# Optimization experiments

Hardware: AMD Instinct MI355X
Metric: run time of the kernel (lower is better)

The kernel has to match this reference:

```python
import jax, jax.numpy as jnp
import numpy as np

NLAT_IN, NLON_IN = 360, 720
NLAT_OUT, NLON_OUT = 180, 360
KERNEL_SIZE = 3
THETA_CUTOFF = KERNEL_SIZE * np.pi / NLAT_IN  # default theta_cutoff
B, C = 2, 64


def _cc_lats_weights(n):
    # Clenshaw-Curtis quadrature on [-1,1] (torch-harmonics 'equiangular' grid);
    # latitudes (colatitude) = arccos(nodes) = pi*k/(n-1) in [0, pi].
    N = n - 1
    theta = np.pi * np.arange(n) / N
    w = np.ones(n)
    for j in range(1, N // 2 + 1):
        b = 1.0 if 2 * j == N else 2.0
        w -= b * np.cos(2.0 * j * theta) / (4.0 * j * j - 1.0)
    w *= 2.0 / N
    w[0] *= 0.5
    w[-1] *= 0.5
    return theta, w


def _precompute_psi():
    # Mirrors _precompute_convolution_tensor + _compute_support_vals_isotropic.
    d_theta = THETA_CUTOFF / KERNEL_SIZE
    lats_in, _ = _cc_lats_weights(NLAT_IN)
    lats_out, _ = _cc_lats_weights(NLAT_OUT)
    phis = np.linspace(0.0, 2.0 * np.pi, NLON_IN)
    alpha = -lats_in[None, :, None].astype(np.float32)   # [1, H, 1]
    beta = phis[None, None, :].astype(np.float32)        # [1, 1, W]
    gamma = lats_out[:, None, None].astype(np.float32)   # [T, 1, 1]
    z = np.cos(alpha) * np.cos(gamma) - np.cos(beta) * np.sin(alpha) * np.sin(gamma)
    with np.errstate(invalid="ignore"):
        theta = np.arccos(z)  # [T, H, W]; nan where |z|>1 (excluded by mask, as in torch)
    segs, lats, lons, vals = [], [], [], []
    for ik in range(KERNEL_SIZE):
        itheta = ik * d_theta
        with np.errstate(invalid="ignore"):
            mask = (np.abs(theta - itheta) < d_theta) & (theta < THETA_CUTOFF)
        t_idx, h_idx, w_idx = np.nonzero(mask)
        segs.append(ik * NLAT_OUT + t_idx)  # fused (kernel, nlat_out) segment id
        lats.append(h_idx)
        lons.append(w_idx)
        vals.append(1.0 - np.abs(theta[mask] - itheta) / d_theta)
    return (np.concatenate(segs).astype(np.int32),
            np.concatenate(lats).astype(np.int32),
            np.concatenate(lons).astype(np.int32),
            np.concatenate(vals).astype(np.float32))


def setup_inputs() -> dict:
    key = jax.random.key(0)
    x = jax.random.normal(key, (B, C, NLAT_IN, NLON_IN), dtype=jnp.float32)
    _, wgl = _cc_lats_weights(NLAT_IN)
    quad_weights = jnp.asarray(2.0 * np.pi * wgl[:, None] / NLON_IN, dtype=jnp.float32)
    seg, lat, lon, val = _precompute_psi()
    return {"x": x, "quad_weights": quad_weights,
            "psi_seg": jnp.asarray(seg), "psi_lat": jnp.asarray(lat),
            "psi_lon": jnp.asarray(lon), "psi_val": jnp.asarray(val)}


def reference(x, quad_weights, psi_seg, psi_lat, psi_lon, psi_val):
    # out[b,c,k,t,p] = sum_{(k,t,h,w) in psi} val * qw[h] * x[b,c,h,(w-(p+1)*s) mod W]
    Bx, Cx, H, W = x.shape
    scale = W // NLON_OUT  # longitudinal shift per output longitude (torch.roll step)
    xw = (quad_weights * x).reshape(Bx * Cx, H, W)  # [BC, H, W]
    num_seg = KERNEL_SIZE * NLAT_OUT

    def step(carry, p):
        cols = (psi_lon - (p + 1) * scale) % W                 # rolled longitude per nnz
        g = xw[:, psi_lat, cols] * psi_val                     # [BC, nnz] gather + scale
        out_p = jax.ops.segment_sum(g.T, psi_seg, num_segments=num_seg)  # [K*T, BC]
        return carry, out_p

    _, ys = jax.lax.scan(step, None, jnp.arange(NLON_OUT))     # [P, K*T, BC]
    out = ys.transpose(2, 1, 0).reshape(Bx, Cx, KERNEL_SIZE, NLAT_OUT, NLON_OUT)
    return out
```

## Files before the change

### kernel.cpp

```cpp
#include <hip/hip_runtime.h>


#define NLAT_IN  360
#define NLON_IN  720
#define NLAT_OUT 180
#define NLON_OUT 360
#define KSIZE    3
#define NSEG     (KSIZE * NLAT_OUT)
#define CHW      (NLAT_IN * NLON_IN)
#define BCTOT    128
#define G        4
#define NBCG     (BCTOT / G)
#define MAXR     2
#define PH       10
#define NTHREADS 256
#define SLOTS    432
#define MIRROR   (SLOTS - NLON_OUT)
#define ROWB     (SLOTS * 16)
#define SWI      3

typedef float v2f __attribute__((ext_vector_type(2)));

__device__ __forceinline__ void PKF(v2f& a, v2f x, v2f c) {
    asm("v_pk_fma_f32 %0, %1, %2, %0" : "+v"(a) : "v"(x), "v"(c));
}


__global__ void prep1_kernel(const int* __restrict__ seg, const int* __restrict__ lat,
                             const float* __restrict__ val, int nnz,
                             int* __restrict__ ptrh, int* __restrict__ hbase,
                             int* __restrict__ hlast, int* __restrict__ flags) {
    int idx = blockIdx.x * blockDim.x + threadIdx.x;
    if (idx >= NSEG * PH) return;
    int s = idx / PH, j = idx - s * PH;
    int lo = 0, hi = nnz;
    while (lo < hi) { int m = (lo + hi) >> 1; if (seg[m] < s) lo = m + 1; else hi = m; }
    int e0 = lo;
    lo = e0; hi = nnz;
    while (lo < hi) { int m = (lo + hi) >> 1; if (seg[m] < s + 1) lo = m + 1; else hi = m; }
    int e1 = lo;
    if (e0 >= e1) {
        ptrh[idx] = e0; flags[idx] = 0;
        if (j == 0) { hbase[s] = 1 << 28; hlast[s] = -(1 << 28); }
        return;
    }
    int hb = lat[e0];
    if (j == 0) { hbase[s] = hb; hlast[s] = lat[e1 - 1]; }
    int a;
    { int tg = hb + j; lo = e0; hi = e1;
      while (lo < hi) { int m = (lo + hi) >> 1; if (lat[m] < tg) lo = m + 1; else hi = m; }
      a = lo; }
    ptrh[idx] = a;
    int f = 0;
    if (j < PH - 1) {
        int tg = hb + j + 1; lo = a; hi = e1;
        while (lo < hi) { int m = (lo + hi) >> 1; if (lat[m] < tg) lo = m + 1; else hi = m; }
        int b = lo;
        if (b - a == NLON_IN) {
            float v0 = val[a], v1 = val[a + 240], v2 = val[a + 480];
            float d = fmaxf(fabsf(v0 - v1), fmaxf(fabsf(v0 - v2), fabsf(v1 - v2)));
            f = (d < 1e-5f) ? 1 : 0;
        }
    }
    flags[idx] = f;
}

__global__ void cf_kernel(const int* __restrict__ lat, const float* __restrict__ val,
                          const float* __restrict__ qw, int nnz, float* __restrict__ cfb) {
    int e = blockIdx.x * blockDim.x + threadIdx.x;
    if (e < nnz) cfb[e] = val[e] * qw[lat[e]];
}

__global__ void runs_kernel(const int* __restrict__ lon, const int* __restrict__ ptrh,
                            const int* __restrict__ flags,
                            int* __restrict__ runcnt, uint2* __restrict__ runslab) {
    const int idx  = blockIdx.x * 4 + (threadIdx.x >> 6);
    if (idx >= NSEG * PH) return;
    const int lane = threadIdx.x & 63;
    const int j = idx % PH;
    int runbase = 0;
    if (j < PH - 1) {
        const int a = ptrh[idx], b = ptrh[idx + 1];
        if (b > a && !flags[idx]) {
            for (int c = a; c < b; c += 64) {
                const int e = c + lane;
                const bool active = e < b;
                const int w   = active ? lon[e] : 0;
                const int wm1 = (active && e > a) ? lon[e - 1] : -99;
                const bool isStart = active && (lane == 0 || w != wm1 + 1);
                const unsigned long long mask = __ballot(isStart);
                if (isStart) {
                    const int cnt = min(64, b - c);
                    unsigned long long hv = (mask >> lane) >> 1;
                    const int len = hv ? __ffsll((long long)hv) : (cnt - lane);
                    const int cidx = __popcll(mask & ((1ull << lane) - 1ull));
                    const int s0 = ((w >> 1) + NLON_OUT - 1) % NLON_OUT;
                    runslab[a + runbase + cidx] = make_uint2(
                        (unsigned)e, (unsigned)(s0 | ((w & 1) << 9) | (len << 11)));
                }
                runbase += __popcll(mask);
            }
        }
    }
    if (lane == 0) runcnt[idx] = runbase;
}


__global__ __launch_bounds__(NTHREADS) void disco_kernel(
    const float* __restrict__ x,
    const float* __restrict__ cfb,
    const uint2* __restrict__ runslab,
    const int*   __restrict__ runcnt,
    const int*   __restrict__ ptrh,
    const int*   __restrict__ hbase,
    const int*   __restrict__ hlast,
    const int*   __restrict__ flags,
    float*       __restrict__ out)
{
    __shared__ float4 ldsx[MAXR * 2][SLOTS];
    __shared__ v2f    accbuf[120][6];

    const int tid      = threadIdx.x;
    const int lane     = tid & 63;
    const int wpair    = tid >> 7;
    const int pairlane = tid & 127;
    const int pid      = (pairlane < 120) ? pairlane : pairlane - 120;
    const int p0       = 3 * pid;
    const int bc0      = blockIdx.x * G;
    const int ty       = blockIdx.y;
    const int t        = (ty & 1) ? (NLAT_OUT - 1 - (ty >> 1)) : (ty >> 1);
    const int s        = blockIdx.z * NLAT_OUT + t;
    const int hb = hbase[s], hl = hlast[s];

    v2f a0l = {0.f, 0.f}, a0h = a0l, a1l = a0l, a1h = a0l, a2l = a0l, a2h = a0l;
    const char* lb = (const char*)&ldsx[0][0];

    float2 sv0[4], sv1[4], sv2[4];
    const float* xb = x + (size_t)bc0 * CHW;

#define LOADW(R0)                                                              \
    {                                                                          \
        {   const int idx_ = tid;                     \
            const int rr_ = idx_ >= 360;                                       \
            const int m_  = idx_ - 360 * rr_;                                  \
            const int row_ = min((R0) + rr_, hl);                              \
            const float* xr_ = xb + (size_t)row_ * NLON_IN + 2 * m_;           \
            sv0[0] = *(const float2*)(xr_);                                    \
            sv0[1] = *(const float2*)(xr_ + CHW);                              \
            sv0[2] = *(const float2*)(xr_ + 2 * CHW);                          \
            sv0[3] = *(const float2*)(xr_ + 3 * CHW);                          \
        }                                                                      \
        {   const int idx_ = tid + 256;               \
            const int rr_ = idx_ >= 360;                                       \
            const int m_  = idx_ - 360 * rr_;                                  \
            const int row_ = min((R0) + rr_, hl);                              \
            const float* xr_ = xb + (size_t)row_ * NLON_IN + 2 * m_;           \
            sv1[0] = *(const float2*)(xr_);                                    \
            sv1[1] = *(const float2*)(xr_ + CHW);                              \
            sv1[2] = *(const float2*)(xr_ + 2 * CHW);                          \
            sv1[3] = *(const float2*)(xr_ + 3 * CHW);                          \
        }                                                                      \
        if (tid < 208) {                                 \
            const int idx_ = tid + 512;                                        \
            const int rr_ = 1;                                                 \
            const int m_  = idx_ - 360;                                        \
            const int row_ = min((R0) + rr_, hl);                              \
            const float* xr_ = xb + (size_t)row_ * NLON_IN + 2 * m_;           \
            sv2[0] = *(const float2*)(xr_);                                    \
            sv2[1] = *(const float2*)(xr_ + CHW);                              \
            sv2[2] = *(const float2*)(xr_ + 2 * CHW);                          \
            sv2[3] = *(const float2*)(xr_ + 3 * CHW);                          \
        }                                                                      \
    }

#define WRITEW()                                                               \
    {                                                                          \
        {   const int idx_ = tid;                                              \
            const int rr_ = idx_ >= 360;                                       \
            const int m_  = idx_ - 360 * rr_;                                  \
            const float4 ev_ = {sv0[0].x, sv0[1].x, sv0[2].x, sv0[3].x};       \
            const float4 ov_ = {sv0[0].y, sv0[1].y, sv0[2].y, sv0[3].y};       \
            ldsx[2 * rr_ + 0][m_] = ev_;                                       \
            ldsx[2 * rr_ + 1][m_] = ov_;                                       \
            if (m_ < MIRROR) {                                                 \
                ldsx[2 * rr_ + 0][NLON_OUT + m_] = ev_;                        \
                ldsx[2 * rr_ + 1][NLON_OUT + m_] = ov_;                        \
            }                                                                  \
        }                                                                      \
        {   const int idx_ = tid + 256;                                        \
            const int rr_ = idx_ >= 360;                                       \
            const int m_  = idx_ - 360 * rr_;                                  \
            const float4 ev_ = {sv1[0].x, sv1[1].x, sv1[2].x, sv1[3].x};       \
            const float4 ov_ = {sv1[0].y, sv1[1].y, sv1[2].y, sv1[3].y};       \
            ldsx[2 * rr_ + 0][m_] = ev_;                                       \
            ldsx[2 * rr_ + 1][m_] = ov_;                                       \
            if (m_ < MIRROR) {                                                 \
                ldsx[2 * rr_ + 0][NLON_OUT + m_] = ev_;                        \
                ldsx[2 * rr_ + 1][NLON_OUT + m_] = ov_;                        \
            }                                                                  \
        }                                                                      \
        if (tid < 208) {                                                       \
            const int m_ = tid + 512 - 360;                                    \
            const float4 ev_ = {sv2[0].x, sv2[1].x, sv2[2].x, sv2[3].x};       \
            const float4 ov_ = {sv2[0].y, sv2[1].y, sv2[2].y, sv2[3].y};       \
            ldsx[2][m_] = ev_;                                                 \
            ldsx[3][m_] = ov_;                                                 \
            if (m_ < MIRROR) {                                                 \
                ldsx[2][NLON_OUT + m_] = ev_;                                  \
                ldsx[3][NLON_OUT + m_] = ov_;                                  \
            }                                                                  \
        }                                                                      \
    }

    if (hb <= hl) {
        LOADW(hb);
        for (int r0 = hb; r0 <= hl; r0 += MAXR) {
            const int rn = min(MAXR, hl - r0 + 1);
            __syncthreads();
            WRITEW();
            if (r0 + MAXR <= hl) LOADW(r0 + MAXR);
            __syncthreads();
            for (int r = 0; r < rn; ++r) {
                const int j = (r0 + r) - hb;
                if (j < 0 || j >= PH - 1) continue;
                if ((j & 1) != wpair) continue;
                const int idx = s * PH + j;
                const int a = ptrh[idx], b = ptrh[idx + 1];
                if (a >= b) continue;
                const int rp0 = (j & 1) * 2;
                if (flags[idx]) {
                    float4 v = {0.f, 0.f, 0.f, 0.f};
                    for (int m = lane; m < NLON_OUT; m += 64) {
                        const float4 u0 = ldsx[rp0][m], u1 = ldsx[rp0 + 1][m];
                        v.x += u0.x + u1.x; v.y += u0.y + u1.y;
                        v.z += u0.z + u1.z; v.w += u0.w + u1.w;
                    }
#pragma unroll
                    for (int o = 32; o >= 1; o >>= 1) {
                        v.x += __shfl_xor(v.x, o); v.y += __shfl_xor(v.y, o);
                        v.z += __shfl_xor(v.z, o); v.w += __shfl_xor(v.w, o);
                    }
                    const float cf = cfb[a];
                    a0l.x = fmaf(cf, v.x, a0l.x); a0l.y = fmaf(cf, v.y, a0l.y);
                    a0h.x = fmaf(cf, v.z, a0h.x); a0h.y = fmaf(cf, v.w, a0h.y);
                    a1l.x = fmaf(cf, v.x, a1l.x); a1l.y = fmaf(cf, v.y, a1l.y);
                    a1h.x = fmaf(cf, v.z, a1h.x); a1h.y = fmaf(cf, v.w, a1h.y);
                    a2l.x = fmaf(cf, v.x, a2l.x); a2l.y = fmaf(cf, v.y, a2l.y);
                    a2h.x = fmaf(cf, v.z, a2h.x); a2h.y = fmaf(cf, v.w, a2h.y);
                    continue;
                }
                const int rc = runcnt[idx];
                for (int rr = 0; rr < rc; ++rr) {
                    const uint2 R = runslab[a + rr];
                    const int e0  = __builtin_amdgcn_readfirstlane((int)R.x);
                    const int y   = __builtin_amdgcn_readfirstlane((int)R.y);
                    const int s0A = y & 511;
                    const int odd = (y >> 9) & 1;
                    const int len = y >> 11;
                    int qA = s0A - p0 - 2; qA += (qA >> 31) & NLON_OUT;
                    const char* baseA = lb + (size_t)(rp0 + odd) * ROWB + ((size_t)qA << 4);
                    const char* baseB = lb + (size_t)(rp0 + (odd ^ 1)) * ROWB
                                           + ((size_t)(qA + odd) << 4);
                    const float* cfp = cfb + e0;
                    int i = 0;
                    if (len >= 8) {
                        v2f A0l = *(const v2f*)(baseA +  0), A0h = *(const v2f*)(baseA +  8);
                        v2f A1l = *(const v2f*)(baseA + 16), A1h = *(const v2f*)(baseA + 24);
                        v2f A2l = *(const v2f*)(baseA + 32), A2h = *(const v2f*)(baseA + 40);
                        v2f B0l = *(const v2f*)(baseB +  0), B0h = *(const v2f*)(baseB +  8);
                        v2f B1l = *(const v2f*)(baseB + 16), B1h = *(const v2f*)(baseB + 24);
                        v2f B2l = *(const v2f*)(baseB + 32), B2h = *(const v2f*)(baseB + 40);
                        v2f A3l, A3h, B3l, B3h;
                        const char* ldA = baseA + 48;
                        const char* ldB = baseB + 48;
                        for (; i + 8 <= len; i += 8) {
                            float cs; v2f c;
                            A3l = *(const v2f*)(ldA); A3h = *(const v2f*)(ldA + 8); ldA += 16;
                            cs = cfp[i + 0]; c = (v2f){cs, cs};
                            PKF(a2l, A0l, c); PKF(a2h, A0h, c);
                            PKF(a1l, A1l, c); PKF(a1h, A1h, c);
                            PKF(a0l, A2l, c); PKF(a0h, A2h, c);
                            B3l = *(const v2f*)(ldB); B3h = *(const v2f*)(ldB + 8); ldB += 16;
                            cs = cfp[i + 1]; c = (v2f){cs, cs};
                            PKF(a2l, B0l, c); PKF(a2h, B0h, c);
                            PKF(a1l, B1l, c); PKF(a1h, B1h, c);
                            PKF(a0l, B2l, c); PKF(a0h, B2h, c);
                            A0l = *(const v2f*)(ldA); A0h = *(const v2f*)(ldA + 8); ldA += 16;
                            cs = cfp[i + 2]; c = (v2f){cs, cs};
                            PKF(a2l, A1l, c); PKF(a2h, A1h, c);
                            PKF(a1l, A2l, c); PKF(a1h, A2h, c);
                            PKF(a0l, A3l, c); PKF(a0h, A3h, c);
                            B0l = *(const v2f*)(ldB); B0h = *(const v2f*)(ldB + 8); ldB += 16;
                            cs = cfp[i + 3]; c = (v2f){cs, cs};
                            PKF(a2l, B1l, c); PKF(a2h, B1h, c);
                            PKF(a1l, B2l, c); PKF(a1h, B2h, c);
                            PKF(a0l, B3l, c); PKF(a0h, B3h, c);
                            A1l = *(const v2f*)(ldA); A1h = *(const v2f*)(ldA + 8); ldA += 16;
                            cs = cfp[i + 4]; c = (v2f){cs, cs};
                            PKF(a2l, A2l, c); PKF(a2h, A2h, c);
                            PKF(a1l, A3l, c); PKF(a1h, A3h, c);
                            PKF(a0l, A0l, c); PKF(a0h, A0h, c);
                            B1l = *(const v2f*)(ldB); B1h = *(const v2f*)(ldB + 8); ldB += 16;
                            cs = cfp[i + 5]; c = (v2f){cs, cs};
                            PKF(a2l, B2l, c); PKF(a2h, B2h, c);
                            PKF(a1l, B3l, c); PKF(a1h, B3h, c);
                            PKF(a0l, B0l, c); PKF(a0h, B0h, c);
                            A2l = *(const v2f*)(ldA); A2h = *(const v2f*)(ldA + 8); ldA += 16;
                            cs = cfp[i + 6]; c = (v2f){cs, cs};
                            PKF(a2l, A3l, c); PKF(a2h, A3h, c);
                            PKF(a1l, A0l, c); PKF(a1h, A0h, c);
                            PKF(a0l, A1l, c); PKF(a0h, A1h, c);
                            B2l = *(const v2f*)(ldB); B2h = *(const v2f*)(ldB + 8); ldB += 16;
                            cs = cfp[i + 7]; c = (v2f){cs, cs};
                            PKF(a2l, B3l, c); PKF(a2h, B3h, c);
                            PKF(a1l, B0l, c); PKF(a1h, B0h, c);
                            PKF(a0l, B1l, c); PKF(a0h, B1h, c);
                        }
                    }
                    for (; i < len; ++i) {
                        const int m = i >> 1;
                        const char* bp = (i & 1) ? (baseB + ((size_t)m << 4))
                                                 : (baseA + ((size_t)m << 4));
                        const float cs = cfp[i]; const v2f c = (v2f){cs, cs};
                        const v2f w0l = *(const v2f*)(bp +  0), w0h = *(const v2f*)(bp +  8);
                        const v2f w1l = *(const v2f*)(bp + 16), w1h = *(const v2f*)(bp + 24);
                        const v2f w2l = *(const v2f*)(bp + 32), w2h = *(const v2f*)(bp + 40);
                        PKF(a2l, w0l, c); PKF(a2h, w0h, c);
                        PKF(a1l, w1l, c); PKF(a1h, w1h, c);
                        PKF(a0l, w2l, c); PKF(a0h, w2h, c);
                    }
                }
            }
        }
    }

    __syncthreads();
    if (wpair == 1 && pairlane < 120) {
        accbuf[pid][0] = a0l; accbuf[pid][1] = a0h;
        accbuf[pid][2] = a1l; accbuf[pid][3] = a1h;
        accbuf[pid][4] = a2l; accbuf[pid][5] = a2h;
    }
    __syncthreads();
    if (wpair == 0 && pairlane < 120) {
        a0l += accbuf[pid][0]; a0h += accbuf[pid][1];
        a1l += accbuf[pid][2]; a1h += accbuf[pid][3];
        a2l += accbuf[pid][4]; a2h += accbuf[pid][5];
        const size_t cs_ = (size_t)NSEG * NLON_OUT;
        const size_t ob  = ((size_t)bc0 * NSEG + s) * NLON_OUT + p0;
        out[ob]              = a0l.x; out[ob + 1]              = a1l.x; out[ob + 2]              = a2l.x;
        out[ob + cs_]        = a0l.y; out[ob + cs_ + 1]        = a1l.y; out[ob + cs_ + 2]        = a2l.y;
        out[ob + 2 * cs_]    = a0h.x; out[ob + 2 * cs_ + 1]    = a1h.x; out[ob + 2 * cs_ + 2]    = a2h.x;
        out[ob + 3 * cs_]    = a0h.y; out[ob + 3 * cs_ + 1]    = a1h.y; out[ob + 3 * cs_ + 2]    = a2h.y;
    }
#undef LOADW
#undef WRITEW
}


__global__ void segptr_kernel(const int* __restrict__ seg, int nnz, int* __restrict__ ptr) {
    int s = blockIdx.x * blockDim.x + threadIdx.x;
    if (s > NSEG) return;
    if (s == NSEG) { ptr[NSEG] = nnz; return; }
    int lo = 0, hi = nnz;
    while (lo < hi) { int m = (lo + hi) >> 1; if (seg[m] < s) lo = m + 1; else hi = m; }
    ptr[s] = lo;
}

__global__ __launch_bounds__(384) void disco_simple_kernel(
    const float* __restrict__ x, const float* __restrict__ qw,
    const int* __restrict__ lat, const int* __restrict__ lon,
    const float* __restrict__ val, const int* __restrict__ ptr,
    float* __restrict__ out)
{
    const int p = threadIdx.x;
    if (p >= NLON_OUT) return;
    const int kt = blockIdx.x, bc0 = blockIdx.y * 8;
    const int e0 = ptr[kt], e1 = ptr[kt + 1];
    float acc[8];
#pragma unroll
    for (int g = 0; g < 8; ++g) acc[g] = 0.0f;
    const int pw = 2 * p + 2;
    const float* xb = x + (size_t)bc0 * CHW;
    for (int e = e0; e < e1; ++e) {
        const int h = lat[e], w = lon[e];
        const float cf = val[e] * qw[h];
        int col = w - pw; if (col < 0) col += NLON_IN;
        const float* src = xb + h * NLON_IN + col;
#pragma unroll
        for (int g = 0; g < 8; ++g) acc[g] = fmaf(cf, src[(size_t)g * CHW], acc[g]);
    }
    const size_t ob = ((size_t)bc0 * NSEG + kt) * NLON_OUT + p;
#pragma unroll
    for (int g = 0; g < 8; ++g) out[ob + (size_t)g * NSEG * NLON_OUT] = acc[g];
}


extern "C" void kernel_launch(void* const* d_in, const int* in_sizes, int n_in,
                              void* d_out, int out_size, void* d_ws, size_t ws_size,
                              hipStream_t stream)
{
    const float* x   = (const float*)d_in[0];
    const float* qw  = (const float*)d_in[1];
    const int*   seg = (const int*)  d_in[2];
    const int*   lat = (const int*)  d_in[3];
    const int*   lon = (const int*)  d_in[4];
    const float* val = (const float*)d_in[5];
    const int    nnz = in_sizes[2];
    const int    nnzpad = (nnz + 3) & ~3;

    char* w = (char*)d_ws;
    size_t off = 0;
    int* ptrh   = (int*)(w + off); off += (size_t)NSEG * PH * 4;
    int* hbase  = (int*)(w + off); off += NSEG * 4;
    int* hlast  = (int*)(w + off); off += NSEG * 4;
    int* flags  = (int*)(w + off); off += (size_t)NSEG * PH * 4;
    int* runcnt = (int*)(w + off); off += (size_t)NSEG * PH * 4;
    float* cfb  = (float*)(w + off); off += (size_t)nnzpad * 4;
    off = (off + 7) & ~(size_t)7;
    uint2* runslab = (uint2*)(w + off); off += (size_t)nnz * 8;

    if (ws_size < off) {
        int* ptr = (int*)d_ws;
        segptr_kernel<<<(NSEG + 1 + 255) / 256, 256, 0, stream>>>(seg, nnz, ptr);
        dim3 grid(NSEG, BCTOT / 8);
        disco_simple_kernel<<<grid, 384, 0, stream>>>(x, qw, lat, lon, val, ptr,
                                                      (float*)d_out);
        return;
    }

    prep1_kernel<<<(NSEG * PH + 255) / 256, 256, 0, stream>>>(seg, lat, val, nnz,
                                                              ptrh, hbase, hlast, flags);
    cf_kernel<<<(nnz + 255) / 256, 256, 0, stream>>>(lat, val, qw, nnz, cfb);
    runs_kernel<<<(NSEG * PH + 3) / 4, 256, 0, stream>>>(lon, ptrh, flags,
                                                         runcnt, runslab);

    dim3 grid(NBCG, NLAT_OUT, KSIZE);
    disco_kernel<<<grid, NTHREADS, 0, stream>>>(x, cfb, runslab, runcnt,
                                                ptrh, hbase, hlast, flags,
                                                (float*)d_out);
}
```

Before: 152.9 us.

## Fuse kernel-size dimension into one block to share staged input rows

Each block now handles all three kernel-radius segments for one output latitude instead of one segment per block, so the x rows loaded into LDS over the union latitude span are reused across all three filters. A new small kernel computes the union row span per output latitude. The LDS accumulation buffer is aliased onto the staging buffer to save shared memory. This triples accumulator registers per thread and serialises three reduction and store phases, which may reduce occupancy in exchange for a third of the global input traffic.

```diff
diff --git a/kernel.cpp b/kernel.cpp
--- a/kernel.cpp
+++ b/kernel.cpp
@@ -17,7 +17,6 @@
 #define SLOTS    432
 #define MIRROR   (SLOTS - NLON_OUT)
 #define ROWB     (SLOTS * 16)
-#define SWI      3
 
 typedef float v2f __attribute__((ext_vector_type(2)));
 
@@ -63,6 +62,19 @@
         }
     }
     flags[idx] = f;
+}
+
+__global__ void span_kernel(const int* __restrict__ hbase, const int* __restrict__ hlast,
+                            int* __restrict__ hbU, int* __restrict__ hlU) {
+    int t = blockIdx.x * blockDim.x + threadIdx.x;
+    if (t >= NLAT_OUT) return;
+    int lo = 1 << 28, hi = -(1 << 28);
+#pragma unroll
+    for (int k = 0; k < KSIZE; ++k) {
+        lo = min(lo, hbase[k * NLAT_OUT + t]);
+        hi = max(hi, hlast[k * NLAT_OUT + t]);
+    }
+    hbU[t] = lo; hlU[t] = hi;
 }
 
 __global__ void cf_kernel(const int* __restrict__ lat, const float* __restrict__ val,
@@ -113,12 +125,14 @@
     const int*   __restrict__ runcnt,
     const int*   __restrict__ ptrh,
     const int*   __restrict__ hbase,
-    const int*   __restrict__ hlast,
     const int*   __restrict__ flags,
+    const int*   __restrict__ hbU,
+    const int*   __restrict__ hlU,
     float*       __restrict__ out)
 {
-    __shared__ float4 ldsx[MAXR * 2][SLOTS];
-    __shared__ v2f    accbuf[120][6];
+    __shared__ float4 smem4[MAXR * 2 * SLOTS];
+    float4 (*ldsx)[SLOTS] = (float4(*)[SLOTS])smem4;
+    v2f    (*accbuf)[6]   = (v2f(*)[6])smem4;
 
     const int tid      = threadIdx.x;
     const int lane     = tid & 63;
@@ -129,42 +143,43 @@
     const int bc0      = blockIdx.x * G;
     const int ty       = blockIdx.y;
     const int t        = (ty & 1) ? (NLAT_OUT - 1 - (ty >> 1)) : (ty >> 1);
-    const int s        = blockIdx.z * NLAT_OUT + t;
-    const int hb = hbase[s], hl = hlast[s];
-
-    v2f a0l = {0.f, 0.f}, a0h = a0l, a1l = a0l, a1h = a0l, a2l = a0l, a2h = a0l;
-    const char* lb = (const char*)&ldsx[0][0];
+
+    const int rlo = hbU[t], rhi = hlU[t];
+    const int hbK0 = hbase[t];
+    const int hbK1 = hbase[NLAT_OUT + t];
+    const int hbK2 = hbase[2 * NLAT_OUT + t];
+
+    v2f acc[KSIZE][6] = {};
+    const char* lb = (const char*)smem4;
 
     float2 sv0[4], sv1[4], sv2[4];
     const float* xb = x + (size_t)bc0 * CHW;
 
 #define LOADW(R0)                                                              \
     {                                                                          \
-        {   const int idx_ = tid;                     \
+        {   const int idx_ = tid;                                              \
             const int rr_ = idx_ >= 360;                                       \
             const int m_  = idx_ - 360 * rr_;                                  \
-            const int row_ = min((R0) + rr_, hl);                              \
+            const int row_ = min((R0) + rr_, rhi);                             \
             const float* xr_ = xb + (size_t)row_ * NLON_IN + 2 * m_;           \
             sv0[0] = *(const float2*)(xr_);                                    \
             sv0[1] = *(const float2*)(xr_ + CHW);                              \
             sv0[2] = *(const float2*)(xr_ + 2 * CHW);                          \
             sv0[3] = *(const float2*)(xr_ + 3 * CHW);                          \
         }                                                                      \
-        {   const int idx_ = tid + 256;               \
+        {   const int idx_ = tid + 256;                                        \
             const int rr_ = idx_ >= 360;                                       \
             const int m_  = idx_ - 360 * rr_;                                  \
-            const int row_ = min((R0) + rr_, hl);                              \
+            const int row_ = min((R0) + rr_, rhi);                             \
             const float* xr_ = xb + (size_t)row_ * NLON_IN + 2 * m_;           \
             sv1[0] = *(const float2*)(xr_);                                    \
             sv1[1] = *(const float2*)(xr_ + CHW);                              \
             sv1[2] = *(const float2*)(xr_ + 2 * CHW);                          \
             sv1[3] = *(const float2*)(xr_ + 3 * CHW);                          \
         }                                                                      \
-        if (tid < 208) {                                 \
-            const int idx_ = tid + 512;                                        \
-            const int rr_ = 1;                                                 \
-            const int m_  = idx_ - 360;                                        \
-            const int row_ = min((R0) + rr_, hl);                              \
+        if (tid < 208) {                                                       \
+            const int m_  = tid + 512 - 360;                                   \
+            const int row_ = min((R0) + 1, rhi);                               \
             const float* xr_ = xb + (size_t)row_ * NLON_IN + 2 * m_;           \
             sv2[0] = *(const float2*)(xr_);                                    \
             sv2[1] = *(const float2*)(xr_ + CHW);                              \
@@ -212,23 +227,113 @@
         }                                                                      \
     }
 
-    if (hb <= hl) {
-        LOADW(hb);
-        for (int r0 = hb; r0 <= hl; r0 += MAXR) {
-            const int rn = min(MAXR, hl - r0 + 1);
+#define PROCRUNS(ASTART, RC, RP0, ACC)                                         \
+    for (int rr = 0; rr < (RC); ++rr) {                                        \
+        const uint2 R = runslab[(ASTART) + rr];                                \
+        const int e0_ = __builtin_amdgcn_readfirstlane((int)R.x);              \
+        const int y_  = __builtin_amdgcn_readfirstlane((int)R.y);              \
+        const int s0A = y_ & 511;                                              \
+        const int odd = (y_ >> 9) & 1;                                         \
+        const int len = y_ >> 11;                                              \
+        int qA = s0A - p0 - 2; qA += (qA >> 31) & NLON_OUT;                    \
+        const char* baseA = lb + (size_t)((RP0) + odd) * ROWB + ((size_t)qA << 4); \
+        const char* baseB = lb + (size_t)((RP0) + (odd ^ 1)) * ROWB            \
+                               + ((size_t)(qA + odd) << 4);                    \
+        const float* cfp = cfb + e0_;                                          \
+        int i = 0;                                                             \
+        if (len >= 8) {                                                        \
+            v2f A0l = *(const v2f*)(baseA +  0), A0h = *(const v2f*)(baseA +  8); \
+            v2f A1l = *(const v2f*)(baseA + 16), A1h = *(const v2f*)(baseA + 24); \
+            v2f A2l = *(const v2f*)(baseA + 32), A2h = *(const v2f*)(baseA + 40); \
+            v2f B0l = *(const v2f*)(baseB +  0), B0h = *(const v2f*)(baseB +  8); \
+            v2f B1l = *(const v2f*)(baseB + 16), B1h = *(const v2f*)(baseB + 24); \
+            v2f B2l = *(const v2f*)(baseB + 32), B2h = *(const v2f*)(baseB + 40); \
+            v2f A3l, A3h, B3l, B3h;                                            \
+            const char* ldA = baseA + 48;                                      \
+            const char* ldB = baseB + 48;                                      \
+            for (; i + 8 <= len; i += 8) {                                     \
+                float cs; v2f c;                                               \
+                A3l = *(const v2f*)(ldA); A3h = *(const v2f*)(ldA + 8); ldA += 16; \
+                cs = cfp[i + 0]; c = (v2f){cs, cs};                            \
+                PKF(ACC[4], A0l, c); PKF(ACC[5], A0h, c);                      \
+                PKF(ACC[2], A1l, c); PKF(ACC[3], A1h, c);                      \
+                PKF(ACC[0], A2l, c); PKF(ACC[1], A2h, c);                      \
+                B3l = *(const v2f*)(ldB); B3h = *(const v2f*)(ldB + 8); ldB += 16; \
+                cs = cfp[i + 1]; c = (v2f){cs, cs};                            \
+                PKF(ACC[4], B0l, c); PKF(ACC[5], B0h, c);                      \
+                PKF(ACC[2], B1l, c); PKF(ACC[3], B1h, c);                      \
+                PKF(ACC[0], B2l, c); PKF(ACC[1], B2h, c);                      \
+                A0l = *(const v2f*)(ldA); A0h = *(const v2f*)(ldA + 8); ldA += 16; \
+                cs = cfp[i + 2]; c = (v2f){cs, cs};                            \
+                PKF(ACC[4], A1l, c); PKF(ACC[5], A1h, c);                      \
+                PKF(ACC[2], A2l, c); PKF(ACC[3], A2h, c);                      \
+                PKF(ACC[0], A3l, c); PKF(ACC[1], A3h, c);                      \
+                B0l = *(const v2f*)(ldB); B0h = *(const v2f*)(ldB + 8); ldB += 16; \
+                cs = cfp[i + 3]; c = (v2f){cs, cs};                            \
+                PKF(ACC[4], B1l, c); PKF(ACC[5], B1h, c);                      \
+                PKF(ACC[2], B2l, c); PKF(ACC[3], B2h, c);                      \
+                PKF(ACC[0], B3l, c); PKF(ACC[1], B3h, c);                      \
+                A1l = *(const v2f*)(ldA); A1h = *(const v2f*)(ldA + 8); ldA += 16; \
+                cs = cfp[i + 4]; c = (v2f){cs, cs};                            \
+                PKF(ACC[4], A2l, c); PKF(ACC[5], A2h, c);                      \
+                PKF(ACC[2], A3l, c); PKF(ACC[3], A3h, c);                      \
+                PKF(ACC[0], A0l, c); PKF(ACC[1], A0h, c);                      \
+                B1l = *(const v2f*)(ldB); B1h = *(const v2f*)(ldB + 8); ldB += 16; \
+                cs = cfp[i + 5]; c = (v2f){cs, cs};                            \
+                PKF(ACC[4], B2l, c); PKF(ACC[5], B2h, c);                      \
+                PKF(ACC[2], B3l, c); PKF(ACC[3], B3h, c);                      \
+                PKF(ACC[0], B0l, c); PKF(ACC[1], B0h, c);                      \
+                A2l = *(const v2f*)(ldA); A2h = *(const v2f*)(ldA + 8); ldA += 16; \
+                cs = cfp[i + 6]; c = (v2f){cs, cs};                            \
+                PKF(ACC[4], A3l, c); PKF(ACC[5], A3h, c);                      \
+                PKF(ACC[2], A0l, c); PKF(ACC[3], A0h, c);                      \
+                PKF(ACC[0], A1l, c); PKF(ACC[1], A1h, c);                      \
+                B2l = *(const v2f*)(ldB); B2h = *(const v2f*)(ldB + 8); ldB += 16; \
+                cs = cfp[i + 7]; c = (v2f){cs, cs};                            \
+                PKF(ACC[4], B3l, c); PKF(ACC[5], B3h, c);                      \
+                PKF(ACC[2], B0l, c); PKF(ACC[3], B0h, c);                      \
+                PKF(ACC[0], B1l, c); PKF(ACC[1], B1h, c);                      \
+            }                                                                  \
+        }                                                                      \
+        for (; i < len; ++i) {                                                 \
+            const int m_ = i >> 1;                                             \
+            const char* bp = (i & 1) ? (baseB + ((size_t)m_ << 4))             \
+                                     : (baseA + ((size_t)m_ << 4));            \
+            const float cs = cfp[i]; const v2f c = (v2f){cs, cs};              \
+            const v2f w0l = *(const v2f*)(bp +  0), w0h = *(const v2f*)(bp +  8); \
+            const v2f w1l = *(const v2f*)(bp + 16), w1h = *(const v2f*)(bp + 24); \
+            const v2f w2l = *(const v2f*)(bp + 32), w2h = *(const v2f*)(bp + 40); \
+            PKF(ACC[4], w0l, c); PKF(ACC[5], w0h, c);                          \
+            PKF(ACC[2], w1l, c); PKF(ACC[3], w1h, c);                          \
+            PKF(ACC[0], w2l, c); PKF(ACC[1], w2h, c);                          \
+        }                                                                      \
+    }
+
+    if (rlo <= rhi) {
+        LOADW(rlo);
+        for (int r0 = rlo; r0 <= rhi; r0 += MAXR) {
+            const int rn = min(MAXR, rhi - r0 + 1);
             __syncthreads();
             WRITEW();
-            if (r0 + MAXR <= hl) LOADW(r0 + MAXR);
+            if (r0 + MAXR <= rhi) LOADW(r0 + MAXR);
             __syncthreads();
             for (int r = 0; r < rn; ++r) {
-                const int j = (r0 + r) - hb;
-                if (j < 0 || j >= PH - 1) continue;
-                if ((j & 1) != wpair) continue;
-                const int idx = s * PH + j;
-                const int a = ptrh[idx], b = ptrh[idx + 1];
-                if (a >= b) continue;
-                const int rp0 = (j & 1) * 2;
-                if (flags[idx]) {
+                if ((r & 1) != wpair) continue;
+                const int row = r0 + r;
+                const int rp0 = r * 2;
+                int aK[KSIZE], bK[KSIZE], fK[KSIZE], rcK[KSIZE];
+                const int hbKs[KSIZE] = {hbK0, hbK1, hbK2};
+#pragma unroll
+                for (int k = 0; k < KSIZE; ++k) {
+                    const int jk = row - hbKs[k];
+                    const int ok = (jk >= 0) && (jk < PH - 1);
+                    const int idxk = (k * NLAT_OUT + t) * PH + (ok ? jk : 0);
+                    aK[k]  = ok ? ptrh[idxk] : 0;
+                    bK[k]  = ok ? ptrh[idxk + 1] : 0;
+                    fK[k]  = (ok && bK[k] > aK[k]) ? flags[idxk] : 0;
+                    rcK[k] = (ok && bK[k] > aK[k] && !fK[k]) ? runcnt[idxk] : 0;
+                }
+                if (fK[0] | fK[1] | fK[2]) {
                     float4 v = {0.f, 0.f, 0.f, 0.f};
                     for (int m = lane; m < NLON_OUT; m += 64) {
                         const float4 u0 = ldsx[rp0][m], u1 = ldsx[rp0 + 1][m];
@@ -240,120 +345,60 @@
                         v.x += __shfl_xor(v.x, o); v.y += __shfl_xor(v.y, o);
                         v.z += __shfl_xor(v.z, o); v.w += __shfl_xor(v.w, o);
                     }
-                    const float cf = cfb[a];
-                    a0l.x = fmaf(cf, v.x, a0l.x); a0l.y = fmaf(cf, v.y, a0l.y);
-                    a0h.x = fmaf(cf, v.z, a0h.x); a0h.y = fmaf(cf, v.w, a0h.y);
-                    a1l.x = fmaf(cf, v.x, a1l.x); a1l.y = fmaf(cf, v.y, a1l.y);
-                    a1h.x = fmaf(cf, v.z, a1h.x); a1h.y = fmaf(cf, v.w, a1h.y);
-                    a2l.x = fmaf(cf, v.x, a2l.x); a2l.y = fmaf(cf, v.y, a2l.y);
-                    a2h.x = fmaf(cf, v.z, a2h.x); a2h.y = fmaf(cf, v.w, a2h.y);
-                    continue;
-                }
-                const int rc = runcnt[idx];
-                for (int rr = 0; rr < rc; ++rr) {
-                    const uint2 R = runslab[a + rr];
-                    const int e0  = __builtin_amdgcn_readfirstlane((int)R.x);
-                    const int y   = __builtin_amdgcn_readfirstlane((int)R.y);
-                    const int s0A = y & 511;
-                    const int odd = (y >> 9) & 1;
-                    const int len = y >> 11;
-                    int qA = s0A - p0 - 2; qA += (qA >> 31) & NLON_OUT;
-                    const char* baseA = lb + (size_t)(rp0 + odd) * ROWB + ((size_t)qA << 4);
-                    const char* baseB = lb + (size_t)(rp0 + (odd ^ 1)) * ROWB
-                                           + ((size_t)(qA + odd) << 4);
-                    const float* cfp = cfb + e0;
-                    int i = 0;
-                    if (len >= 8) {
-                        v2f A0l = *(const v2f*)(baseA +  0), A0h = *(const v2f*)(baseA +  8);
-                        v2f A1l = *(const v2f*)(baseA + 16), A1h = *(const v2f*)(baseA + 24);
-                        v2f A2l = *(const v2f*)(baseA + 32), A2h = *(const v2f*)(baseA + 40);
-                        v2f B0l = *(const v2f*)(baseB +  0), B0h = *(const v2f*)(baseB +  8);
-                        v2f B1l = *(const v2f*)(baseB + 16), B1h = *(const v2f*)(baseB + 24);
-                        v2f B2l = *(const v2f*)(baseB + 32), B2h = *(const v2f*)(baseB + 40);
-                        v2f A3l, A3h, B3l, B3h;
-                        const char* ldA = baseA + 48;
-                        const char* ldB = baseB + 48;
-                        for (; i + 8 <= len; i += 8) {
-                            float cs; v2f c;
-                            A3l = *(const v2f*)(ldA); A3h = *(const v2f*)(ldA + 8); ldA += 16;
-                            cs = cfp[i + 0]; c = (v2f){cs, cs};
-                            PKF(a2l, A0l, c); PKF(a2h, A0h, c);
-                            PKF(a1l, A1l, c); PKF(a1h, A1h, c);
-                            PKF(a0l, A2l, c); PKF(a0h, A2h, c);
-                            B3l = *(const v2f*)(ldB); B3h = *(const v2f*)(ldB + 8); ldB += 16;
-                            cs = cfp[i + 1]; c = (v2f){cs, cs};
-                            PKF(a2l, B0l, c); PKF(a2h, B0h, c);
-                            PKF(a1l, B1l, c); PKF(a1h, B1h, c);
-                            PKF(a0l, B2l, c); PKF(a0h, B2h, c);
-                            A0l = *(const v2f*)(ldA); A0h = *(const v2f*)(ldA + 8); ldA += 16;
-                            cs = cfp[i + 2]; c = (v2f){cs, cs};
-                            PKF(a2l, A1l, c); PKF(a2h, A1h, c);
-                            PKF(a1l, A2l, c); PKF(a1h, A2h, c);
-                            PKF(a0l, A3l, c); PKF(a0h, A3h, c);
-                            B0l = *(const v2f*)(ldB); B0h = *(const v2f*)(ldB + 8); ldB += 16;
-                            cs = cfp[i + 3]; c = (v2f){cs, cs};
-                            PKF(a2l, B1l, c); PKF(a2h, B1h, c);
-                            PKF(a1l, B2l, c); PKF(a1h, B2h, c);
-                            PKF(a0l, B3l, c); PKF(a0h, B3h, c);
-                            A1l = *(const v2f*)(ldA); A1h = *(const v2f*)(ldA + 8); ldA += 16;
-                            cs = cfp[i + 4]; c = (v2f){cs, cs};
-                            PKF(a2l, A2l, c); PKF(a2h, A2h, c);
-                            PKF(a1l, A3l, c); PKF(a1h, A3h, c);
-                            PKF(a0l, A0l, c); PKF(a0h, A0h, c);
-                            B1l = *(const v2f*)(ldB); B1h = *(const v2f*)(ldB + 8); ldB += 16;
-                            cs = cfp[i + 5]; c = (v2f){cs, cs};
-                            PKF(a2l, B2l, c); PKF(a2h, B2h, c);
-                            PKF(a1l, B3l, c); PKF(a1h, B3h, c);
-                            PKF(a0l, B0l, c); PKF(a0h, B0h, c);
-                            A2l = *(const v2f*)(ldA); A2h = *(const v2f*)(ldA + 8); ldA += 16;
-                            cs = cfp[i + 6]; c = (v2f){cs, cs};
-                            PKF(a2l, A3l, c); PKF(a2h, A3h, c);
-                            PKF(a1l, A0l, c); PKF(a1h, A0h, c);
-                            PKF(a0l, A1l, c); PKF(a0h, A1h, c);
-                            B2l = *(const v2f*)(ldB); B2h = *(const v2f*)(ldB + 8); ldB += 16;
-                            cs = cfp[i + 7]; c = (v2f){cs, cs};
-                            PKF(a2l, B3l, c); PKF(a2h, B3h, c);
-                            PKF(a1l, B0l, c); PKF(a1h, B0h, c);
-                            PKF(a0l, B1l, c); PKF(a0h, B1h, c);
+#pragma unroll
+                    for (int k = 0; k < KSIZE; ++k) {
+                        if (fK[k]) {
+                            const float cf = cfb[aK[k]];
+                            acc[k][0].x = fmaf(cf, v.x, acc[k][0].x);
+                            acc[k][0].y = fmaf(cf, v.y, acc[k][0].y);
+                            acc[k][1].x = fmaf(cf, v.z, acc[k][1].x);
+                            acc[k][1].y = fmaf(cf, v.w, acc[k][1].y);
+                            acc[k][2].x = fmaf(cf, v.x, acc[k][2].x);
+                            acc[k][2].y = fmaf(cf, v.y, acc[k][2].y);
+                            acc[k][3].x = fmaf(cf, v.z, acc[k][3].x);
+                            acc[k][3].y = fmaf(cf, v.w, acc[k][3].y);
+                            acc[k][4].x = fmaf(cf, v.x, acc[k][4].x);
+                            acc[k][4].y = fmaf(cf, v.y, acc[k][4].y);
+                            acc[k][5].x = fmaf(cf, v.z, acc[k][5].x);
+                            acc[k][5].y = fmaf(cf, v.w, acc[k][5].y);
                         }
                     }
-                    for (; i < len; ++i) {
-                        const int m = i >> 1;
-                        const char* bp = (i & 1) ? (baseB + ((size_t)m << 4))
-                                                 : (baseA + ((size_t)m << 4));
-                        const float cs = cfp[i]; const v2f c = (v2f){cs, cs};
-                        const v2f w0l = *(const v2f*)(bp +  0), w0h = *(const v2f*)(bp +  8);
-                        const v2f w1l = *(const v2f*)(bp + 16), w1h = *(const v2f*)(bp + 24);
-                        const v2f w2l = *(const v2f*)(bp + 32), w2h = *(const v2f*)(bp + 40);
-                        PKF(a2l, w0l, c); PKF(a2h, w0h, c);
-                        PKF(a1l, w1l, c); PKF(a1h, w1h, c);
-                        PKF(a0l, w2l, c); PKF(a0h, w2h, c);
-                    }
+                }
+#pragma unroll
+                for (int k = 0; k < KSIZE; ++k) {
+                    if (rcK[k] > 0) { PROCRUNS(aK[k], rcK[k], rp0, acc[k]); }
                 }
             }
         }
     }
 
-    __syncthreads();
-    if (wpair == 1 && pairlane < 120) {
-        accbuf[pid][0] = a0l; accbuf[pid][1] = a0h;
-        accbuf[pid][2] = a1l; accbuf[pid][3] = a1h;
-        accbuf[pid][4] = a2l; accbuf[pid][5] = a2h;
-    }
-    __syncthreads();
-    if (wpair == 0 && pairlane < 120) {
-        a0l += accbuf[pid][0]; a0h += accbuf[pid][1];
-        a1l += accbuf[pid][2]; a1h += accbuf[pid][3];
-        a2l += accbuf[pid][4]; a2h += accbuf[pid][5];
-        const size_t cs_ = (size_t)NSEG * NLON_OUT;
-        const size_t ob  = ((size_t)bc0 * NSEG + s) * NLON_OUT + p0;
-        out[ob]              = a0l.x; out[ob + 1]              = a1l.x; out[ob + 2]              = a2l.x;
-        out[ob + cs_]        = a0l.y; out[ob + cs_ + 1]        = a1l.y; out[ob + cs_ + 2]        = a2l.y;
-        out[ob + 2 * cs_]    = a0h.x; out[ob + 2 * cs_ + 1]    = a1h.x; out[ob + 2 * cs_ + 2]    = a2h.x;
-        out[ob + 3 * cs_]    = a0h.y; out[ob + 3 * cs_ + 1]    = a1h.y; out[ob + 3 * cs_ + 2]    = a2h.y;
+    const size_t cs_ = (size_t)NSEG * NLON_OUT;
+#pragma unroll
+    for (int k = 0; k < KSIZE; ++k) {
+        __syncthreads();
+        if (wpair == 1 && pairlane < 120) {
+            accbuf[pid][0] = acc[k][0]; accbuf[pid][1] = acc[k][1];
+            accbuf[pid][2] = acc[k][2]; accbuf[pid][3] = acc[k][3];
+            accbuf[pid][4] = acc[k][4]; accbuf[pid][5] = acc[k][5];
+        }
+        __syncthreads();
+        if (wpair == 0 && pairlane < 120) {
+            const v2f b0 = accbuf[pid][0], b1 = accbuf[pid][1];
+            const v2f b2 = accbuf[pid][2], b3 = accbuf[pid][3];
+            const v2f b4 = accbuf[pid][4], b5 = accbuf[pid][5];
+            const v2f r0_ = acc[k][0] + b0, r1_ = acc[k][1] + b1;
+            const v2f r2_ = acc[k][2] + b2, r3_ = acc[k][3] + b3;
+            const v2f r4_ = acc[k][4] + b4, r5_ = acc[k][5] + b5;
+            const size_t ob = ((size_t)bc0 * NSEG + k * NLAT_OUT + t) * NLON_OUT + p0;
+            out[ob]              = r0_.x; out[ob + 1]              = r2_.x; out[ob + 2]              = r4_.x;
+            out[ob + cs_]        = r0_.y; out[ob + cs_ + 1]        = r2_.y; out[ob + cs_ + 2]        = r4_.y;
+            out[ob + 2 * cs_]    = r1_.x; out[ob + 2 * cs_ + 1]    = r3_.x; out[ob + 2 * cs_ + 2]    = r5_.x;
+            out[ob + 3 * cs_]    = r1_.y; out[ob + 3 * cs_ + 1]    = r3_.y; out[ob + 3 * cs_ + 2]    = r5_.y;
+        }
     }
 #undef LOADW
 #undef WRITEW
+#undef PROCRUNS
 }
 
 
@@ -415,6 +460,8 @@
     int* hlast  = (int*)(w + off); off += NSEG * 4;
     int* flags  = (int*)(w + off); off += (size_t)NSEG * PH * 4;
     int* runcnt = (int*)(w + off); off += (size_t)NSEG * PH * 4;
+    int* hbU    = (int*)(w + off); off += NLAT_OUT * 4;
+    int* hlU    = (int*)(w + off); off += NLAT_OUT * 4;
     float* cfb  = (float*)(w + off); off += (size_t)nnzpad * 4;
     off = (off + 7) & ~(size_t)7;
     uint2* runslab = (uint2*)(w + off); off += (size_t)nnz * 8;
@@ -430,12 +477,13 @@
 
     prep1_kernel<<<(NSEG * PH + 255) / 256, 256, 0, stream>>>(seg, lat, val, nnz,
                                                               ptrh, hbase, hlast, flags);
+    span_kernel<<<1, 256, 0, stream>>>(hbase, hlast, hbU, hlU);
     cf_kernel<<<(nnz + 255) / 256, 256, 0, stream>>>(lat, val, qw, nnz, cfb);
     runs_kernel<<<(NSEG * PH + 3) / 4, 256, 0, stream>>>(lon, ptrh, flags,
                                                          runcnt, runslab);
 
-    dim3 grid(NBCG, NLAT_OUT, KSIZE);
+    dim3 grid(NBCG, NLAT_OUT);
     disco_kernel<<<grid, NTHREADS, 0, stream>>>(x, cfb, runslab, runcnt,
-                                                ptrh, hbase, hlast, flags,
+                                                ptrh, hbase, flags, hbU, hlU,
                                                 (float*)d_out);
 }
```

Measured after the change: 166.1 us. 8.6% more time.
